# Performance work log

Measured on AMD Instinct MI355X. Metric: run time of the kernel, lower is better.

## Reference

```python
import jax, jax.numpy as jnp
import numpy as np

N_NODES = 100000
N_EDGES = 1600000
IN_CH, HID_CH, OUT_CH = 512, 128, 128


def gcn_conv(x, src, dst, deg_isqrt, W, b, n_nodes):
    # PyG GCNConv: linear transform, then symmetric-normalized scatter-add
    h = x @ W  # [N, F_out]
    norm = deg_isqrt[src] * deg_isqrt[dst]  # [E+N]
    msg = h[src] * norm[:, None]  # gather + scale
    out = jax.ops.segment_sum(msg, dst, num_segments=n_nodes)
    return out + b


def setup_inputs() -> dict:
    key = jax.random.key(0)
    k1, k2, k3, k4 = jax.random.split(key, 4)
    x = jax.random.normal(k1, (N_NODES, IN_CH), dtype=jnp.float32)
    edge_index = jax.random.randint(k2, (2, N_EDGES), 0, N_NODES, dtype=jnp.int64)
    # Glorot-ish init for weights
    W1 = jax.random.normal(k3, (IN_CH, HID_CH), dtype=jnp.float32) / np.sqrt(IN_CH)
    W2 = jax.random.normal(k4, (HID_CH, OUT_CH), dtype=jnp.float32) / np.sqrt(HID_CH)
    b1 = jnp.zeros((HID_CH,), dtype=jnp.float32)
    b2 = jnp.zeros((OUT_CH,), dtype=jnp.float32)
    return {"x": x, "edge_index": edge_index, "W1": W1, "b1": b1, "W2": W2, "b2": b2}


def reference(x, edge_index, W1, b1, W2, b2):
    n_nodes = x.shape[0]
    # add self-loops (PyG default add_self_loops=True)
    loops = jnp.arange(n_nodes, dtype=edge_index.dtype)
    src = jnp.concatenate([edge_index[0], loops])
    dst = jnp.concatenate([edge_index[1], loops])
    # degree (in-degree over edges incl. self-loops), shared by both layers
    deg = jax.ops.segment_sum(jnp.ones_like(dst, dtype=x.dtype), dst, num_segments=n_nodes)
    deg_isqrt = jax.lax.rsqrt(deg)  # deg >= 1 thanks to self-loops
    h = gcn_conv(x, src, dst, deg_isqrt, W1, b1, n_nodes)
    h = jax.nn.relu(h)
    out = gcn_conv(h, src, dst, deg_isqrt, W2, b2, n_nodes)
    return out
```

## Files before the change

kernel.cpp:

```cpp
#include <hip/hip_runtime.h>
#include <hip/hip_bf16.h>

#define CH 128
#define IN_CH_K 512
#define CHUNK 2048
#define BPAD 5120

typedef short s16x8 __attribute__((ext_vector_type(8)));
typedef float f32x4 __attribute__((ext_vector_type(4)));

__device__ __forceinline__ unsigned int f2bf(float f) {
    unsigned int u = __builtin_bit_cast(unsigned int, f);
    return (u + 0x7fffu + ((u >> 16) & 1u)) >> 16;
}
__device__ __forceinline__ unsigned int pk2bf(float lo, float hi) {
    unsigned int r;
    asm("v_cvt_pk_bf16_f32 %0, %1, %2" : "=v"(r) : "v"(lo), "v"(hi));
    return r;
}
__device__ __forceinline__ float bf_lo(unsigned int u) {
    return __builtin_bit_cast(float, u << 16);
}
__device__ __forceinline__ float bf_hi(unsigned int u) {
    return __builtin_bit_cast(float, u & 0xFFFF0000u);
}
__device__ __forceinline__ unsigned int relu_pk(unsigned int w) {
    unsigned int keep = (~w) & 0x80008000u;
    unsigned int mask = keep - (keep >> 15);
    return w & mask;
}

__global__ void init_cursor_kernel(int* __restrict__ cursor, int NB) {
    int i = blockIdx.x * blockDim.x + threadIdx.x;
    if (i < NB) cursor[i] = i * BPAD;
}

__global__ void bin_kernel(const int* __restrict__ src, const int* __restrict__ dst,
                           int* __restrict__ cursor, int* __restrict__ binned,
                           int E, int NB) {
    __shared__ int h[512];
    __shared__ int base[512];
    __shared__ int cur[512];
    const int tid = threadIdx.x;
    for (int i = tid; i < NB; i += 256) h[i] = 0;
    __syncthreads();

    const int E4 = E >> 2;
    const int beg4 = blockIdx.x * (CHUNK / 4);
    const int end4 = min(E4, beg4 + CHUNK / 4);
    const int4* dst4 = reinterpret_cast<const int4*>(dst);
    const int4* src4 = reinterpret_cast<const int4*>(src);
    const bool last = (blockIdx.x == gridDim.x - 1);

    for (int e4 = beg4 + tid; e4 < end4; e4 += 256) {
        int4 d = dst4[e4];
        atomicAdd(&h[d.x >> 8], 1);
        atomicAdd(&h[d.y >> 8], 1);
        atomicAdd(&h[d.z >> 8], 1);
        atomicAdd(&h[d.w >> 8], 1);
    }
    if (last) {
        for (int e = (E & ~3) + tid; e < E; e += 256)
            atomicAdd(&h[dst[e] >> 8], 1);
    }
    __syncthreads();
    for (int i = tid; i < NB; i += 256) {
        cur[i] = 0;
        if (h[i]) base[i] = atomicAdd(&cursor[i], h[i]);
    }
    __syncthreads();

    for (int e4 = beg4 + tid; e4 < end4; e4 += 256) {
        int4 d = dst4[e4];
        int4 s = src4[e4];
        int b, r, idx;
        b = d.x >> 8; r = atomicAdd(&cur[b], 1); idx = base[b] + r;
        if (idx < (b + 1) * BPAD) binned[idx] = s.x | ((d.x & 255) << 17);
        b = d.y >> 8; r = atomicAdd(&cur[b], 1); idx = base[b] + r;
        if (idx < (b + 1) * BPAD) binned[idx] = s.y | ((d.y & 255) << 17);
        b = d.z >> 8; r = atomicAdd(&cur[b], 1); idx = base[b] + r;
        if (idx < (b + 1) * BPAD) binned[idx] = s.z | ((d.z & 255) << 17);
        b = d.w >> 8; r = atomicAdd(&cur[b], 1); idx = base[b] + r;
        if (idx < (b + 1) * BPAD) binned[idx] = s.w | ((d.w & 255) << 17);
    }
    if (last) {
        for (int e = (E & ~3) + tid; e < E; e += 256) {
            int d = dst[e];
            int b = d >> 8;
            int r = atomicAdd(&cur[b], 1);
            int idx = base[b] + r;
            if (idx < (b + 1) * BPAD) binned[idx] = src[e] | ((d & 255) << 17);
        }
    }
}

__global__ void csr_bucket_kernel(const int* __restrict__ binned, const int* __restrict__ cursor,
                                  int2* __restrict__ row_range, int* __restrict__ csr_src,
                                  float* __restrict__ dinv, int N) {
    __shared__ int cnt[256];
    __shared__ int off[256];
    __shared__ int cur[256];
    const int k = blockIdx.x;
    const int t = threadIdx.x;
    cnt[t] = 0;
    __syncthreads();
    const int beg = k * BPAD;
    const int end = min(cursor[k], (k + 1) * BPAD);
    const int nv = (end - beg) & ~3;
    const int4* b4 = reinterpret_cast<const int4*>(binned + beg);

    for (int q = t; q * 4 < nv; q += 256) {
        int4 p = b4[q];
        atomicAdd(&cnt[p.x >> 17], 1);
        atomicAdd(&cnt[p.y >> 17], 1);
        atomicAdd(&cnt[p.z >> 17], 1);
        atomicAdd(&cnt[p.w >> 17], 1);
    }
    for (int e = beg + nv + t; e < end; e += 256)
        atomicAdd(&cnt[binned[e] >> 17], 1);
    __syncthreads();
    int v = cnt[t];
    off[t] = v;
    __syncthreads();
    #pragma unroll
    for (int o = 1; o < 256; o <<= 1) {
        int tv = (t >= o) ? off[t - o] : 0;
        __syncthreads();
        off[t] += tv;
        __syncthreads();
    }
    int ex = off[t] - v;
    int node = k * 256 + t;
    if (node < N) {
        row_range[node] = make_int2(beg + ex, beg + ex + v);
        dinv[node] = rsqrtf((float)(v + 1));
    }
    cur[t] = ex;
    __syncthreads();
    for (int q = t; q * 4 < nv; q += 256) {
        int4 p = b4[q];
        int dl, r;
        dl = p.x >> 17; r = atomicAdd(&cur[dl], 1); csr_src[beg + r] = p.x & 0x1FFFF;
        dl = p.y >> 17; r = atomicAdd(&cur[dl], 1); csr_src[beg + r] = p.y & 0x1FFFF;
        dl = p.z >> 17; r = atomicAdd(&cur[dl], 1); csr_src[beg + r] = p.z & 0x1FFFF;
        dl = p.w >> 17; r = atomicAdd(&cur[dl], 1); csr_src[beg + r] = p.w & 0x1FFFF;
    }
    for (int e = beg + nv + t; e < end; e += 256) {
        int p = binned[e];
        int dl = p >> 17;
        int r = atomicAdd(&cur[dl], 1);
        csr_src[beg + r] = p & 0x1FFFF;
    }
}

template<bool PERM>
__global__ void convert_w_kernel(const float* __restrict__ W, uint4* __restrict__ WT, int K) {
    int i = blockIdx.x * blockDim.x + threadIdx.x;
    int ng = K >> 3;
    if (i >= ng * CH) return;
    int g = i >> 7;
    int col = i & 127;
    unsigned int h[8];
    #pragma unroll
    for (int j = 0; j < 8; ++j) {
        int kp = g * 8 + j;
        int k = PERM ? ((kp >> 3) + ((kp & 7) << 4)) : kp;
        h[j] = f2bf(W[(size_t)k * CH + col]);
    }
    uint4 v;
    v.x = h[0] | (h[1] << 16);
    v.y = h[2] | (h[3] << 16);
    v.z = h[4] | (h[5] << 16);
    v.w = h[6] | (h[7] << 16);
    WT[i] = v;
}

__launch_bounds__(256)
__global__ void gemm1_mfma_kernel(const float* __restrict__ A, const uint4* __restrict__ WT,
                                  const float* __restrict__ dinv, unsigned short* __restrict__ C,
                                  int M) {
    const int tid = threadIdx.x;
    const int wid = tid >> 6;
    const int lane = tid & 63;
    const int l15 = lane & 15;
    const int lg = lane >> 4;

    const int block_row = blockIdx.x * 128 + wid * 32;

    f32x4 acc[2][8];
    #pragma unroll
    for (int m = 0; m < 2; ++m)
        #pragma unroll
        for (int n = 0; n < 8; ++n)
            acc[m][n] = (f32x4){0.f, 0.f, 0.f, 0.f};

    const int arow0 = min(block_row + l15, M - 1);
    const int arow1 = min(block_row + 16 + l15, M - 1);
    const float4* ap0 = reinterpret_cast<const float4*>(A + (size_t)arow0 * IN_CH_K) + lg * 2;
    const float4* ap1 = reinterpret_cast<const float4*>(A + (size_t)arow1 * IN_CH_K) + lg * 2;
    const uint4* wp = WT + (size_t)lg * CH + l15;

    float4 a00 = ap0[0], a01 = ap0[1];
    float4 a10 = ap1[0], a11 = ap1[1];
    uint4 bw[8];
    #pragma unroll
    for (int n = 0; n < 8; ++n) bw[n] = wp[n * 16];

    #pragma unroll
    for (int ks = 0; ks < 16; ++ks) {
        float4 na00, na01, na10, na11;
        uint4 nbw[8];
        if (ks < 15) {
            const int o4 = (ks + 1) * 8;
            na00 = ap0[o4];     na01 = ap0[o4 + 1];
            na10 = ap1[o4];     na11 = ap1[o4 + 1];
            const uint4* nwp = wp + (size_t)(ks + 1) * 4 * CH;
            #pragma unroll
            for (int n = 0; n < 8; ++n) nbw[n] = nwp[n * 16];
        }

        uint4 pk0, pk1;
        pk0.x = pk2bf(a00.x, a00.y);  pk0.y = pk2bf(a00.z, a00.w);
        pk0.z = pk2bf(a01.x, a01.y);  pk0.w = pk2bf(a01.z, a01.w);
        pk1.x = pk2bf(a10.x, a10.y);  pk1.y = pk2bf(a10.z, a10.w);
        pk1.z = pk2bf(a11.x, a11.y);  pk1.w = pk2bf(a11.z, a11.w);
        s16x8 af0 = __builtin_bit_cast(s16x8, pk0);
        s16x8 af1 = __builtin_bit_cast(s16x8, pk1);

        #pragma unroll
        for (int n = 0; n < 8; ++n) {
            s16x8 b = __builtin_bit_cast(s16x8, bw[n]);
            acc[0][n] = __builtin_amdgcn_mfma_f32_16x16x32_bf16(af0, b, acc[0][n], 0, 0, 0);
            acc[1][n] = __builtin_amdgcn_mfma_f32_16x16x32_bf16(af1, b, acc[1][n], 0, 0, 0);
        }

        if (ks < 15) {
            a00 = na00; a01 = na01; a10 = na10; a11 = na11;
            #pragma unroll
            for (int n = 0; n < 8; ++n) bw[n] = nbw[n];
        }
    }

    #pragma unroll
    for (int m = 0; m < 2; ++m) {
        #pragma unroll
        for (int i = 0; i < 4; ++i) {
            int row = block_row + m * 16 + lg * 4 + i;
            if (row < M) {
                float s = dinv[row];
                uint4 v;
                v.x = pk2bf(acc[m][0][i] * s, acc[m][1][i] * s);
                v.y = pk2bf(acc[m][2][i] * s, acc[m][3][i] * s);
                v.z = pk2bf(acc[m][4][i] * s, acc[m][5][i] * s);
                v.w = pk2bf(acc[m][6][i] * s, acc[m][7][i] * s);
                *reinterpret_cast<uint4*>(&C[(size_t)row * CH + l15 * 8]) = v;
            }
        }
    }
}

__launch_bounds__(256)
__global__ void gemm2_mfma_kernel(const unsigned short* __restrict__ A, const uint4* __restrict__ WT,
                                  const float* __restrict__ dinv, unsigned short* __restrict__ C,
                                  int M) {
    const int tid = threadIdx.x;
    const int wid = tid >> 6;
    const int lane = tid & 63;
    const int l15 = lane & 15;
    const int lg = lane >> 4;

    const int block_row = blockIdx.x * 128 + wid * 32;

    f32x4 acc[2][8];
    #pragma unroll
    for (int m = 0; m < 2; ++m)
        #pragma unroll
        for (int n = 0; n < 8; ++n)
            acc[m][n] = (f32x4){0.f, 0.f, 0.f, 0.f};

    int arow0 = min(block_row + l15, M - 1);
    int arow1 = min(block_row + 16 + l15, M - 1);
    const uint4* ap0 = reinterpret_cast<const uint4*>(A + (size_t)arow0 * CH);
    const uint4* ap1 = reinterpret_cast<const uint4*>(A + (size_t)arow1 * CH);

    #pragma unroll
    for (int k0 = 0; k0 < CH; k0 += 32) {
        const int fi = (k0 >> 3) + lg;
        uint4 r0 = ap0[fi];
        uint4 r1 = ap1[fi];
        r0.x = relu_pk(r0.x); r0.y = relu_pk(r0.y); r0.z = relu_pk(r0.z); r0.w = relu_pk(r0.w);
        r1.x = relu_pk(r1.x); r1.y = relu_pk(r1.y); r1.z = relu_pk(r1.z); r1.w = relu_pk(r1.w);
        s16x8 a0 = __builtin_bit_cast(s16x8, r0);
        s16x8 a1 = __builtin_bit_cast(s16x8, r1);
        #pragma unroll
        for (int n = 0; n < 8; ++n) {
            uint4 bv = WT[(size_t)fi * CH + n * 16 + l15];
            s16x8 b = __builtin_bit_cast(s16x8, bv);
            acc[0][n] = __builtin_amdgcn_mfma_f32_16x16x32_bf16(a0, b, acc[0][n], 0, 0, 0);
            acc[1][n] = __builtin_amdgcn_mfma_f32_16x16x32_bf16(a1, b, acc[1][n], 0, 0, 0);
        }
    }

    #pragma unroll
    for (int m = 0; m < 2; ++m) {
        #pragma unroll
        for (int i = 0; i < 4; ++i) {
            int row = block_row + m * 16 + lg * 4 + i;
            if (row < M) {
                float s = dinv[row];
                uint4 v;
                v.x = pk2bf(acc[m][0][i] * s, acc[m][1][i] * s);
                v.y = pk2bf(acc[m][2][i] * s, acc[m][3][i] * s);
                v.z = pk2bf(acc[m][4][i] * s, acc[m][5][i] * s);
                v.w = pk2bf(acc[m][6][i] * s, acc[m][7][i] * s);
                *reinterpret_cast<uint4*>(&C[(size_t)row * CH + l15 * 8]) = v;
            }
        }
    }
}

#define GATHER(cc) g[(size_t)__builtin_amdgcn_readfirstlane(cc) * 64 + lane]
template<bool OUT_BF16>
__launch_bounds__(256)
__global__ void aggregate_kernel(const unsigned int* __restrict__ g, const int2* __restrict__ row_range,
                                 const int* __restrict__ csr_src, const float* __restrict__ dinv,
                                 const float* __restrict__ bias, void* __restrict__ outp, int N) {
    const int gtid = blockIdx.x * blockDim.x + threadIdx.x;
    const int node = gtid >> 6;
    if (node >= N) return;
    const int lane = threadIdx.x & 63;

    unsigned int su = g[(size_t)node * 64 + lane];
    const int2 rr = row_range[node];
    float ax = bf_lo(su);
    float ay = bf_hi(su);

    int j = rr.x;
    const int end = rr.y;

    if (j + 8 <= end) {
        int c0 = csr_src[j], c1 = csr_src[j+1], c2 = csr_src[j+2], c3 = csr_src[j+3];
        int c4 = csr_src[j+4], c5 = csr_src[j+5], c6 = csr_src[j+6], c7 = csr_src[j+7];
        j += 8;
        while (j + 8 <= end) {
            int n0 = csr_src[j], n1 = csr_src[j+1], n2 = csr_src[j+2], n3 = csr_src[j+3];
            int n4 = csr_src[j+4], n5 = csr_src[j+5], n6 = csr_src[j+6], n7 = csr_src[j+7];
            j += 8;
            unsigned int u0 = GATHER(c0), u1 = GATHER(c1), u2 = GATHER(c2), u3 = GATHER(c3);
            unsigned int u4 = GATHER(c4), u5 = GATHER(c5), u6 = GATHER(c6), u7 = GATHER(c7);
            ax += ((bf_lo(u0) + bf_lo(u1)) + (bf_lo(u2) + bf_lo(u3)))
                + ((bf_lo(u4) + bf_lo(u5)) + (bf_lo(u6) + bf_lo(u7)));
            ay += ((bf_hi(u0) + bf_hi(u1)) + (bf_hi(u2) + bf_hi(u3)))
                + ((bf_hi(u4) + bf_hi(u5)) + (bf_hi(u6) + bf_hi(u7)));
            c0 = n0; c1 = n1; c2 = n2; c3 = n3;
            c4 = n4; c5 = n5; c6 = n6; c7 = n7;
        }
        unsigned int u0 = GATHER(c0), u1 = GATHER(c1), u2 = GATHER(c2), u3 = GATHER(c3);
        unsigned int u4 = GATHER(c4), u5 = GATHER(c5), u6 = GATHER(c6), u7 = GATHER(c7);
        ax += ((bf_lo(u0) + bf_lo(u1)) + (bf_lo(u2) + bf_lo(u3)))
            + ((bf_lo(u4) + bf_lo(u5)) + (bf_lo(u6) + bf_lo(u7)));
        ay += ((bf_hi(u0) + bf_hi(u1)) + (bf_hi(u2) + bf_hi(u3)))
            + ((bf_hi(u4) + bf_hi(u5)) + (bf_hi(u6) + bf_hi(u7)));
    }
    for (; j + 2 <= end; j += 2) {
        int c0 = csr_src[j], c1 = csr_src[j+1];
        unsigned int u0 = GATHER(c0), u1 = GATHER(c1);
        ax += bf_lo(u0) + bf_lo(u1);
        ay += bf_hi(u0) + bf_hi(u1);
    }
    if (j < end) {
        int c0 = csr_src[j];
        unsigned int u0 = GATHER(c0);
        ax += bf_lo(u0);
        ay += bf_hi(u0);
    }

    const int cp0 = lane << 1;
    const int cp1 = cp0 | 1;
    const int c0 = (cp0 >> 3) + ((cp0 & 7) << 4);
    const int c1 = (cp1 >> 3) + ((cp1 & 7) << 4);
    const float di = dinv[node];
    float ox = di * ax + bias[c0];
    float oy = di * ay + bias[c1];
    if (OUT_BF16) {
        ((unsigned int*)outp)[(size_t)node * 64 + lane] = pk2bf(ox, oy);
    } else {
        float* o = (float*)outp + (size_t)node * CH;
        o[c0] = ox;
        o[c1] = oy;
    }
}

extern "C" void kernel_launch(void* const* d_in, const int* in_sizes, int n_in,
                              void* d_out, int out_size, void* d_ws, size_t ws_size,
                              hipStream_t stream) {
    const float* x  = (const float*)d_in[0];
    const int*   ei = (const int*)d_in[1];
    const float* W1 = (const float*)d_in[2];
    const float* b1 = (const float*)d_in[3];
    const float* W2 = (const float*)d_in[4];
    const float* b2 = (const float*)d_in[5];
    float* out = (float*)d_out;

    const int N = in_sizes[0] / IN_CH_K;
    const int E = in_sizes[1] / 2;
    const int* e_src = ei;
    const int* e_dst = ei + E;

    const int NB = (N + 255) >> 8;
    const int NCHUNK = (E + CHUNK - 1) / CHUNK;

    char* w = (char*)d_ws;
    auto alloc = [&](size_t bytes) {
        char* p = w;
        w += (bytes + 255) & ~(size_t)255;
        return p;
    };
    int*   cursor    = (int*)  alloc((size_t)NB * 4);
    int2*  row_range = (int2*) alloc((size_t)N * 8);
    float* dinv      = (float*)alloc((size_t)N * 4);
    int*   csr_src   = (int*)  alloc((size_t)NB * BPAD * 4);
    uint4* w1t       = (uint4*)alloc((size_t)(IN_CH_K / 8) * CH * 16);
    uint4* w2t       = (uint4*)alloc((size_t)(CH / 8) * CH * 16);
    unsigned short* gbuf = (unsigned short*)alloc((size_t)N * CH * 2);
    unsigned short* abuf = (unsigned short*)alloc((size_t)N * CH * 2);
    int* binned = (int*)gbuf;

    init_cursor_kernel<<<(NB + 255) / 256, 256, 0, stream>>>(cursor, NB);
    bin_kernel<<<NCHUNK, 256, 0, stream>>>(e_src, e_dst, cursor, binned, E, NB);
    csr_bucket_kernel<<<NB, 256, 0, stream>>>(binned, cursor, row_range, csr_src, dinv, N);
    convert_w_kernel<false><<<(IN_CH_K / 8 * CH + 255) / 256, 256, 0, stream>>>(W1, w1t, IN_CH_K);
    convert_w_kernel<true><<<(CH / 8 * CH + 255) / 256, 256, 0, stream>>>(W2, w2t, CH);

    const int gemm_grid = (N + 127) / 128;
    const int agg_grid = (N * 64 + 255) / 256;

    gemm1_mfma_kernel<<<gemm_grid, 256, 0, stream>>>(x, w1t, dinv, gbuf, N);
    aggregate_kernel<true><<<agg_grid, 256, 0, stream>>>((const unsigned int*)gbuf, row_range,
                                                         csr_src, dinv, b1, abuf, N);

    gemm2_mfma_kernel<<<gemm_grid, 256, 0, stream>>>(abuf, w2t, dinv, gbuf, N);
    aggregate_kernel<false><<<agg_grid, 256, 0, stream>>>((const unsigned int*)gbuf, row_range,
                                                          csr_src, dinv, b2, out, N);
}
```

Before: 276.7 us.

## Restructure gemm1 to 16 rows per wave with full A-row prefetch

gemm1 now has each wave handle 16 rows instead of 32, and loads the whole 512-float A row slice for all 16 k-steps into registers up front, so every x load is in flight at once rather than double-buffered one step at a time. The grid doubles to 64 rows per block, and launch bounds ask for 2 blocks per CU. The aim is more memory-level parallelism on the bandwidth-bound read of x. The cost is reading the W tiles twice as often per output row and higher register pressure from the 128-float A buffer.

Result: slower. 290.7 us (+5.0%).

```diff
diff --git a/kernel.cpp b/kernel.cpp
--- a/kernel.cpp
+++ b/kernel.cpp
@@ -175,7 +175,7 @@
     WT[i] = v;
 }
 
-__launch_bounds__(256)
+__launch_bounds__(256, 2)
 __global__ void gemm1_mfma_kernel(const float* __restrict__ A, const uint4* __restrict__ WT,
                                   const float* __restrict__ dinv, unsigned short* __restrict__ C,
                                   int M) {
@@ -185,76 +185,65 @@
     const int l15 = lane & 15;
     const int lg = lane >> 4;
 
-    const int block_row = blockIdx.x * 128 + wid * 32;
-
-    f32x4 acc[2][8];
-    #pragma unroll
-    for (int m = 0; m < 2; ++m)
-        #pragma unroll
-        for (int n = 0; n < 8; ++n)
-            acc[m][n] = (f32x4){0.f, 0.f, 0.f, 0.f};
-
-    const int arow0 = min(block_row + l15, M - 1);
-    const int arow1 = min(block_row + 16 + l15, M - 1);
-    const float4* ap0 = reinterpret_cast<const float4*>(A + (size_t)arow0 * IN_CH_K) + lg * 2;
-    const float4* ap1 = reinterpret_cast<const float4*>(A + (size_t)arow1 * IN_CH_K) + lg * 2;
+    const int wave_row = blockIdx.x * 64 + wid * 16;
+    const int arow = min(wave_row + l15, M - 1);
+    const float4* ap = reinterpret_cast<const float4*>(A + (size_t)arow * IN_CH_K) + lg * 2;
+
+    float4 a[16][2];
+    #pragma unroll
+    for (int ks = 0; ks < 16; ++ks) {
+        a[ks][0] = ap[ks * 8];
+        a[ks][1] = ap[ks * 8 + 1];
+    }
+
     const uint4* wp = WT + (size_t)lg * CH + l15;
-
-    float4 a00 = ap0[0], a01 = ap0[1];
-    float4 a10 = ap1[0], a11 = ap1[1];
     uint4 bw[8];
     #pragma unroll
     for (int n = 0; n < 8; ++n) bw[n] = wp[n * 16];
 
+    f32x4 acc[8];
+    #pragma unroll
+    for (int n = 0; n < 8; ++n) acc[n] = (f32x4){0.f, 0.f, 0.f, 0.f};
+
     #pragma unroll
     for (int ks = 0; ks < 16; ++ks) {
-        float4 na00, na01, na10, na11;
         uint4 nbw[8];
         if (ks < 15) {
-            const int o4 = (ks + 1) * 8;
-            na00 = ap0[o4];     na01 = ap0[o4 + 1];
-            na10 = ap1[o4];     na11 = ap1[o4 + 1];
             const uint4* nwp = wp + (size_t)(ks + 1) * 4 * CH;
             #pragma unroll
             for (int n = 0; n < 8; ++n) nbw[n] = nwp[n * 16];
         }
 
-        uint4 pk0, pk1;
-        pk0.x = pk2bf(a00.x, a00.y);  pk0.y = pk2bf(a00.z, a00.w);
-        pk0.z = pk2bf(a01.x, a01.y);  pk0.w = pk2bf(a01.z, a01.w);
-        pk1.x = pk2bf(a10.x, a10.y);  pk1.y = pk2bf(a10.z, a10.w);
-        pk1.z = pk2bf(a11.x, a11.y);  pk1.w = pk2bf(a11.z, a11.w);
-        s16x8 af0 = __builtin_bit_cast(s16x8, pk0);
-        s16x8 af1 = __builtin_bit_cast(s16x8, pk1);
+        uint4 pk;
+        pk.x = pk2bf(a[ks][0].x, a[ks][0].y);
+        pk.y = pk2bf(a[ks][0].z, a[ks][0].w);
+        pk.z = pk2bf(a[ks][1].x, a[ks][1].y);
+        pk.w = pk2bf(a[ks][1].z, a[ks][1].w);
+        s16x8 af = __builtin_bit_cast(s16x8, pk);
 
         #pragma unroll
         for (int n = 0; n < 8; ++n) {
             s16x8 b = __builtin_bit_cast(s16x8, bw[n]);
-            acc[0][n] = __builtin_amdgcn_mfma_f32_16x16x32_bf16(af0, b, acc[0][n], 0, 0, 0);
-            acc[1][n] = __builtin_amdgcn_mfma_f32_16x16x32_bf16(af1, b, acc[1][n], 0, 0, 0);
+            acc[n] = __builtin_amdgcn_mfma_f32_16x16x32_bf16(af, b, acc[n], 0, 0, 0);
         }
 
         if (ks < 15) {
-            a00 = na00; a01 = na01; a10 = na10; a11 = na11;
             #pragma unroll
             for (int n = 0; n < 8; ++n) bw[n] = nbw[n];
         }
     }
 
     #pragma unroll
-    for (int m = 0; m < 2; ++m) {
-        #pragma unroll
-        for (int i = 0; i < 4; ++i) {
-            int row = block_row + m * 16 + lg * 4 + i;
-            if (row < M) {
-                float s = dinv[row];
-                uint4 v;
-                v.x = pk2bf(acc[m][0][i] * s, acc[m][1][i] * s);
-                v.y = pk2bf(acc[m][2][i] * s, acc[m][3][i] * s);
-                v.z = pk2bf(acc[m][4][i] * s, acc[m][5][i] * s);
-                v.w = pk2bf(acc[m][6][i] * s, acc[m][7][i] * s);
-                *reinterpret_cast<uint4*>(&C[(size_t)row * CH + l15 * 8]) = v;
-            }
+    for (int i = 0; i < 4; ++i) {
+        int row = wave_row + lg * 4 + i;
+        if (row < M) {
+            float s = dinv[row];
+            uint4 v;
+            v.x = pk2bf(acc[0][i] * s, acc[1][i] * s);
+            v.y = pk2bf(acc[2][i] * s, acc[3][i] * s);
+            v.z = pk2bf(acc[4][i] * s, acc[5][i] * s);
+            v.w = pk2bf(acc[6][i] * s, acc[7][i] * s);
+            *reinterpret_cast<uint4*>(&C[(size_t)row * CH + l15 * 8]) = v;
         }
     }
 }
@@ -432,14 +421,15 @@
     convert_w_kernel<false><<<(IN_CH_K / 8 * CH + 255) / 256, 256, 0, stream>>>(W1, w1t, IN_CH_K);
     convert_w_kernel<true><<<(CH / 8 * CH + 255) / 256, 256, 0, stream>>>(W2, w2t, CH);
 
-    const int gemm_grid = (N + 127) / 128;
+    const int gemm1_grid = (N + 63) / 64;
+    const int gemm2_grid = (N + 127) / 128;
     const int agg_grid = (N * 64 + 255) / 256;
 
-    gemm1_mfma_kernel<<<gemm_grid, 256, 0, stream>>>(x, w1t, dinv, gbuf, N);
+    gemm1_mfma_kernel<<<gemm1_grid, 256, 0, stream>>>(x, w1t, dinv, gbuf, N);
     aggregate_kernel<true><<<agg_grid, 256, 0, stream>>>((const unsigned int*)gbuf, row_range,
                                                          csr_src, dinv, b1, abuf, N);
 
-    gemm2_mfma_kernel<<<gemm_grid, 256, 0, stream>>>(abuf, w2t, dinv, gbuf, N);
+    gemm2_mfma_kernel<<<gemm2_grid, 256, 0, stream>>>(abuf, w2t, dinv, gbuf, N);
     aggregate_kernel<false><<<agg_grid, 256, 0, stream>>>((const unsigned int*)gbuf, row_range,
                                                           csr_src, dinv, b2, out, N);
 }
```
